# Optimization experiments

Measured on AMD Instinct MI355X. Metric: run time of the kernel, lower is better.

The kernel has to match this reference:

```python
import math
import jax, jax.numpy as jnp
import numpy as np

C = 64
GRID = 2

def _conv1x1(x, W, b):
    # 1x1 conv == channel-mixing matmul: [B,C,H,W] x [O,C] -> [B,O,H,W]
    return jnp.einsum('bchw,oc->bohw', x, W) + b[None, :, None, None]

def setup_inputs() -> dict:
    key = jax.random.key(0)
    ks = jax.random.split(key, 11)
    s = 1.0 / math.sqrt(C)
    def w(k):
        return jax.random.normal(k, (C, C), dtype=jnp.float32) * s
    def bias(k):
        return jax.random.normal(k, (C,), dtype=jnp.float32) * 0.02
    return {
        'x': jax.random.normal(ks[0], (2, C, 128, 128), dtype=jnp.float32),
        'Wq': w(ks[1]), 'bq': bias(ks[2]),
        'Wk': w(ks[3]), 'bk': bias(ks[4]),
        'Wa': w(ks[5]), 'ba': bias(ks[6]),
        'Wb': w(ks[7]), 'bb': bias(ks[8]),
        'Wo': w(ks[9]), 'bo': bias(ks[10]),
    }

def reference(x, Wq, bq, Wk, bk, Wa, ba, Wb, bb, Wo, bo):
    B, c, H, W = x.shape
    g = GRID
    rh, rw = H // g, W // g  # H,W chosen divisible by grid -> no reflect pad
    N = rh * rw
    R = g * g

    q = _conv1x1(x, Wq, bq)
    k = _conv1x1(x, Wk, bk)
    a = _conv1x1(x, Wa, ba)
    bt = _conv1x1(x, Wb, bb)

    def regionize(t):
        # [B,C,H,W] -> [B, R, C, N] with N = rh*rw row-major per region
        return t.reshape(B, c, g, rh, g, rw).transpose(0, 2, 4, 1, 3, 5).reshape(B, R, c, N)

    qr, kr, ar, br = regionize(q), regionize(k), regionize(a), regionize(bt)

    # attn[b,r,n,m] = softmax_m( q^T k / sqrt(C) )
    attn = jax.nn.softmax(jnp.einsum('brcn,brcm->brnm', qr, kr) / math.sqrt(c), axis=-1)

    # out_r = alpha @ attn + beta @ attn^T
    out = (jnp.einsum('brcj,brjm->brcm', ar, attn)
           + jnp.einsum('brcj,brmj->brcm', br, attn))

    # [B,R,C,N] -> [B,C,H,W]
    out = out.reshape(B, g, g, c, rh, rw).transpose(0, 3, 1, 4, 2, 5).reshape(B, c, H, W)
    return _conv1x1(out, Wo, bo)
```

## Files before the change

kernel.cpp:

```cpp
#include <hip/hip_runtime.h>


typedef __attribute__((ext_vector_type(8)))  short bf16x8;
typedef __attribute__((ext_vector_type(16))) float f32x16;

#define MFMA32(a, b, c) __builtin_amdgcn_mfma_f32_32x32x16_bf16(a, b, c, 0, 0, 0)

constexpr int REG_ELEMS = 4096 * 64;
constexpr size_t QP_OFF  = 0;
constexpr size_t KP_OFF  = 4u  << 20;
constexpr size_t ATL_OFF = 8u  << 20;
constexpr size_t BTL_OFF = 12u << 20;
constexpr size_t OUTP_OFF= 16u << 20;
constexpr size_t LNV_OFF = 20u << 20;

constexpr float QSCALE = 0.18033688011112042f;

__device__ __forceinline__ short f2bf(float f) {
    union { float f; unsigned u; } v; v.f = f;
    unsigned r = v.u + 0x7fffu + ((v.u >> 16) & 1u);
    return (short)(r >> 16);
}
__device__ __forceinline__ float bf2f(short s) {
    union { unsigned u; float f; } v; v.u = ((unsigned)(unsigned short)s) << 16;
    return v.f;
}
__device__ __forceinline__ unsigned fbits(float f) {
    union { float f; unsigned u; } v; v.f = f; return v.u;
}
__device__ __forceinline__ unsigned pack_trunc(float e0, float e1) {
    return __builtin_amdgcn_perm(fbits(e1), fbits(e0), 0x07060302u);
}
__device__ __forceinline__ f32x16 zero16() {
    f32x16 z;
    #pragma unroll
    for (int i = 0; i < 16; ++i) z[i] = 0.f;
    return z;
}
__device__ __forceinline__ float fexp2(float x) {
#if __has_builtin(__builtin_amdgcn_exp2f)
    return __builtin_amdgcn_exp2f(x);
#else
    return exp2f(x);
#endif
}
__device__ __forceinline__ void permswap32(unsigned& a, unsigned& b, bool hi) {
#if __has_builtin(__builtin_amdgcn_permlane32_swap)
    auto r = __builtin_amdgcn_permlane32_swap(a, b, false, false);
    a = r[0]; b = r[1];
#elif __has_builtin(__builtin_amdgcn_permlane32_swap_b32)
    auto r = __builtin_amdgcn_permlane32_swap_b32(a, b, false, false);
    a = r[0]; b = r[1];
#else
    unsigned ax = (unsigned)__shfl_xor((int)a, 32);
    unsigned bx = (unsigned)__shfl_xor((int)b, 32);
    unsigned na = hi ? bx : a;
    unsigned nb = hi ? b  : ax;
    a = na; b = nb;
#endif
}

typedef __attribute__((address_space(1))) const unsigned char as1_t;
typedef __attribute__((address_space(3))) unsigned char as3_t;
__device__ __forceinline__ void stage16(const void* g, void* l) {
    __builtin_amdgcn_global_load_lds((as1_t*)g, (as3_t*)l, 16, 0, 0);
}

__global__ __launch_bounds__(256) void k_conv_in(
    const float* __restrict__ x,
    const float* __restrict__ Wq, const float* __restrict__ bq,
    const float* __restrict__ Wk, const float* __restrict__ bk,
    const float* __restrict__ Wa, const float* __restrict__ ba,
    const float* __restrict__ Wb, const float* __restrict__ bb,
    char* __restrict__ ws)
{
    const int tid  = threadIdx.x;
    const int blk  = blockIdx.x;
    const int wseg = blk & 1;
    const int h    = (blk >> 1) & 127;
    const int b    = blk >> 8;
    const int br   = b * 4 + (h >> 6) * 2 + wseg;
    const int n0   = (h & 63) * 64;

    __shared__ float xs[64][68];
    __shared__ short trans[2][64][72];

    const float* xp = x + ((size_t)b * 64 * 16384) + (size_t)h * 128 + wseg * 64;
    #pragma unroll
    for (int r = 0; r < 4; ++r) {
        int idx = r * 256 + tid;
        int c   = idx >> 4;
        int w4  = (idx & 15) << 2;
        *(float4*)&xs[c][w4] = *(const float4*)(xp + (size_t)c * 16384 + w4);
    }
    __syncthreads();

    const int lane = tid & 63;
    const int wid  = tid >> 6;
    const int col  = lane & 31;
    const int l5   = lane >> 5;
    const int pH   = wid & 1;
    const int oH   = wid >> 1;
    const int px   = pH * 32 + col;
    const int oc   = oH * 32 + col;

    bf16x8 xhi[4], xlo[4];
    #pragma unroll
    for (int s = 0; s < 4; ++s) {
        union { bf16x8 v; short sh[8]; } uh, ul;
        #pragma unroll
        for (int e = 0; e < 8; ++e) {
            float xv = xs[s * 16 + l5 * 8 + e][px];
            short hh = f2bf(xv);
            uh.sh[e] = hh;
            ul.sh[e] = f2bf(xv - bf2f(hh));
        }
        xhi[s] = uh.v; xlo[s] = ul.v;
    }

    #pragma unroll
    for (int mat = 0; mat < 4; ++mat) {
        const float* Wsel = (mat == 0) ? Wq : (mat == 1) ? Wk : (mat == 2) ? Wa : Wb;
        const float* bsel = (mat == 0) ? bq : (mat == 1) ? bk : (mat == 2) ? ba : bb;

        bf16x8 whi[4], wlo[4];
        const float* wrow = Wsel + (size_t)oc * 64;
        #pragma unroll
        for (int s = 0; s < 4; ++s) {
            float4 f0 = *(const float4*)(wrow + s * 16 + l5 * 8);
            float4 f1 = *(const float4*)(wrow + s * 16 + l5 * 8 + 4);
            float wf[8] = { f0.x, f0.y, f0.z, f0.w, f1.x, f1.y, f1.z, f1.w };
            union { bf16x8 v; short sh[8]; } uh, ul;
            #pragma unroll
            for (int e = 0; e < 8; ++e) {
                short hh = f2bf(wf[e]);
                uh.sh[e] = hh;
                ul.sh[e] = f2bf(wf[e] - bf2f(hh));
            }
            whi[s] = uh.v; wlo[s] = ul.v;
        }

        f32x16 d = zero16();
        #pragma unroll
        for (int s = 0; s < 4; ++s) {
            d = MFMA32(xhi[s], whi[s], d);
            d = MFMA32(xhi[s], wlo[s], d);
            d = MFMA32(xlo[s], whi[s], d);
        }

        const float bias = bsel[oc];
        if (mat < 2) {
            const float sc = (mat == 0) ? QSCALE : 1.0f;
            #pragma unroll
            for (int r = 0; r < 16; ++r) {
                int pxl = pH * 32 + (r & 3) + 8 * (r >> 2) + 4 * l5;
                trans[mat][pxl][oc] = f2bf((d[r] + bias) * sc);
            }
        } else {
            short* base = (short*)(ws + (mat == 2 ? ATL_OFF : BTL_OFF))
                          + (size_t)br * REG_ELEMS;
            const int sw   = (oc >> 1) & 3;
            const int tile = (n0 >> 5) + pH;
            #pragma unroll
            for (int q = 0; q < 4; ++q) {
                short tmp4[4];
                #pragma unroll
                for (int rr = 0; rr < 4; ++rr) tmp4[rr] = f2bf(d[4 * q + rr] + bias);
                int segp = q ^ sw;
                short* p = base + (size_t)tile * 2048 + oc * 32 + segp * 8 + 4 * l5;
                *(uint2*)p = *(uint2*)tmp4;
            }
        }
    }
    __syncthreads();

    #pragma unroll
    for (int rep = 0; rep < 4; ++rep) {
        int idx  = rep * 256 + tid;
        int mat2 = idx >> 9;
        int row  = (idx >> 3) & 63;
        int seg  = idx & 7;
        short* dst = (short*)(ws + (mat2 ? KP_OFF : QP_OFF))
                     + (size_t)br * REG_ELEMS + (size_t)(n0 + row) * 64
                     + (seg ^ (row & 7)) * 8;
        *(uint4*)dst = *(uint4*)&trans[mat2][row][seg * 8];
    }
}

__global__ __launch_bounds__(256, 2) void k_stats(char* __restrict__ ws)
{
    const int tid  = threadIdx.x;
    const int br   = blockIdx.x & 7;
    const int nt   = blockIdx.x >> 3;
    const int lane = tid & 63;
    const int w    = tid >> 6;
    const int wn   = w & 1;
    const int wi   = w >> 1;
    const int col  = lane & 31;
    const int l5   = lane >> 5;

    const short* Qb  = (const short*)(ws + QP_OFF) + (size_t)br * REG_ELEMS;
    const char*  Kbb = ws + KP_OFF + (size_t)br * REG_ELEMS * 2;

    __shared__ __align__(16) char smem[17408];

    const int nrow = nt * 64 + wn * 32 + col;
    bf16x8 afr[4];
    #pragma unroll
    for (int s = 0; s < 4; ++s)
        afr[s] = *(const bf16x8*)(Qb + (size_t)nrow * 64 + (((2*s+l5) ^ (col & 7)) * 8));

    float sm[16];
    #pragma unroll
    for (int r = 0; r < 16; ++r) sm[r] = 0.f;

    {
        const char* g = Kbb + (size_t)w * 2048 + lane * 16;
        char* l = smem + w * 2048;
        stage16(g, l); stage16(g + 1024, l + 1024);
    }

    #pragma unroll 2
    for (int slab = 0; slab < 64; ++slab) {
        __syncthreads();
        if (slab + 1 < 64) {
            const char* g = Kbb + (size_t)(slab + 1) * 8192 + w * 2048 + lane * 16;
            char* l = smem + ((slab + 1) & 1) * 8192 + w * 2048;
            stage16(g, l); stage16(g + 1024, l + 1024);
        }
        const short* Ks = (const short*)(smem + (slab & 1) * 8192);
        f32x16 d = zero16();
        #pragma unroll
        for (int s = 0; s < 4; ++s) {
            bf16x8 bf = *(const bf16x8*)(Ks + (wi * 32 + col) * 64
                                         + ((2*s+l5) ^ (col & 7)) * 8);
            d = MFMA32(afr[s], bf, d);
        }
        #pragma unroll
        for (int r = 0; r < 16; ++r) sm[r] += fexp2(d[r]);
    }

    #pragma unroll
    for (int off = 1; off < 32; off <<= 1)
        #pragma unroll
        for (int r = 0; r < 16; ++r) sm[r] += __shfl_xor(sm[r], off);

    __syncthreads();
    float* Lred = (float*)(smem + 16384);
    float* Larr = (float*)(smem + 16896);
    if (col == 0) {
        #pragma unroll
        for (int r = 0; r < 16; ++r)
            Lred[w * 32 + ((r & 3) + 8 * (r >> 2) + 4 * l5)] = sm[r];
    }
    __syncthreads();
    if (tid < 64) {
        int wn2 = tid >> 5, nl = tid & 31;
        float L = Lred[wn2 * 32 + nl] + Lred[(wn2 + 2) * 32 + nl];
        float li = 1.0f / L;
        Larr[tid] = li;
        ((float*)(ws + LNV_OFF))[(size_t)br * 4096 + nt * 64 + tid] = li;
    }
    __syncthreads();

    short* Ab = (short*)(ws + ATL_OFF) + (size_t)br * REG_ELEMS + (size_t)nt * 4096;
    #pragma unroll
    for (int rep = 0; rep < 2; ++rep) {
        int id = rep * 256 + tid;
        int t = id >> 8, c = (id >> 2) & 63, s = id & 3;
        int sg = s ^ ((c >> 1) & 3);
        int jl = t * 32 + sg * 8;
        short* p = Ab + (size_t)t * 2048 + c * 32 + s * 8;
        uint4 v = *(uint4*)p;
        short* sp = (short*)&v;
        short o[8];
        #pragma unroll
        for (int e = 0; e < 8; ++e) o[e] = f2bf(bf2f(sp[e]) * Larr[jl + e]);
        *(uint4*)p = *(uint4*)o;
    }
}

__global__ __launch_bounds__(256, 2) void k_attn(char* __restrict__ ws)
{
    const int tid  = threadIdx.x;
    const int br   = blockIdx.x & 7;
    const int mt   = blockIdx.x >> 3;
    const int lane = tid & 63;
    const int w    = tid >> 6;
    const int wm   = w & 1;
    const int wj   = w >> 1;
    const int col  = lane & 31;
    const int l5   = lane >> 5;
    const bool hi  = (l5 != 0);

    const char* Qbb = ws + QP_OFF  + (size_t)br * REG_ELEMS * 2;
    const char* Kbb = ws + KP_OFF  + (size_t)br * REG_ELEMS * 2;
    const char* Abb = ws + ATL_OFF + (size_t)br * REG_ELEMS * 2;
    const char* Bbb = ws + BTL_OFF + (size_t)br * REG_ELEMS * 2;
    const float* Lnv = (const float*)(ws + LNV_OFF) + (size_t)br * 4096;
    short* OutPb    = (short*)(ws + OUTP_OFF) + (size_t)br * REG_ELEMS;

    __shared__ __align__(16) char smem[32768];

    const int mrow = mt * 64 + wm * 32 + col;
    const short* msrc = (const short*)(wj == 0 ? Kbb : Qbb) + (size_t)mrow * 64;
    bf16x8 mf[4];
    #pragma unroll
    for (int s = 0; s < 4; ++s)
        mf[s] = *(const bf16x8*)(msrc + ((2*s+l5) ^ (col & 7)) * 8);

    f32x16 accL = zero16(), accH = zero16();

    const char* gsb = (w == 0) ? Qbb : (w == 1) ? Kbb : (w == 2) ? Abb : Bbb;

    {
        const char* g = gsb + lane * 16;
        char* l = smem + w * 4096 + lane * 16;
        #pragma unroll
        for (int i = 0; i < 4; ++i) stage16(g + i * 1024, l + i * 1024);
    }

    #pragma unroll 2
    for (int slab = 0; slab < 128; ++slab) {
        __syncthreads();
        if (slab + 1 < 128) {
            const char* g = gsb + (size_t)(slab + 1) * 4096 + lane * 16;
            char* l = smem + ((slab + 1) & 1) * 16384 + w * 4096 + lane * 16;
            #pragma unroll
            for (int i = 0; i < 4; ++i) stage16(g + i * 1024, l + i * 1024);
        }
        const char* sb = smem + (slab & 1) * 16384;
        const short* js = (const short*)(sb + (wj == 0 ? 0 : 4096));
        const short* ts = (const short*)(sb + (wj == 0 ? 8192 : 12288));

        f32x16 d = zero16();
        #pragma unroll
        for (int s = 0; s < 4; ++s) {
            bf16x8 a = *(const bf16x8*)(js + col * 64 + ((2*s+l5) ^ (col & 7)) * 8);
            d = MFMA32(a, mf[s], d);
        }

        unsigned Wp[8];
        #pragma unroll
        for (int q = 0; q < 4; ++q) {
            Wp[2*q]   = pack_trunc(fexp2(d[4*q]),   fexp2(d[4*q+1]));
            Wp[2*q+1] = pack_trunc(fexp2(d[4*q+2]), fexp2(d[4*q+3]));
        }

        #pragma unroll
        for (int k16 = 0; k16 < 2; ++k16) {
            unsigned u0 = Wp[4*k16+0], u1 = Wp[4*k16+1];
            unsigned u2 = Wp[4*k16+2], u3 = Wp[4*k16+3];
            permswap32(u0, u2, hi);
            permswap32(u1, u3, hi);
            union { uint4 u; bf16x8 v; } fr;
            fr.u.x = u0; fr.u.y = u1; fr.u.z = u2; fr.u.w = u3;

            const int swz = ((2*k16 + l5) ^ ((col >> 1) & 3)) * 8;
            bf16x8 bL = *(const bf16x8*)(ts + col * 32 + swz);
            bf16x8 bH = *(const bf16x8*)(ts + (col + 32) * 32 + swz);
            accL = MFMA32(fr.v, bL, accL);
            accH = MFMA32(fr.v, bH, accH);
        }
    }

    __syncthreads();
    float* red = (float*)smem;
    if (wj == 0) {
        #pragma unroll
        for (int r = 0; r < 16; ++r) {
            int ml = wm * 32 + (r & 3) + 8 * (r >> 2) + 4 * l5;
            red[ml * 68 + col]      = accL[r];
            red[ml * 68 + 32 + col] = accH[r];
        }
    }
    __syncthreads();
    if (wj == 1) {
        #pragma unroll
        for (int r = 0; r < 16; ++r) {
            int ml = wm * 32 + (r & 3) + 8 * (r >> 2) + 4 * l5;
            float li = Lnv[mt * 64 + ml];
            red[ml * 68 + col]      += li * accL[r];
            red[ml * 68 + 32 + col] += li * accH[r];
        }
    }
    __syncthreads();
    {
        const int m  = tid >> 2;
        const int c0 = (tid & 3) * 16;
        const float* rp = red + m * 68 + c0;
        uint4 p0, p1;
        p0.x = pack_trunc(rp[0],  rp[1]);  p0.y = pack_trunc(rp[2],  rp[3]);
        p0.z = pack_trunc(rp[4],  rp[5]);  p0.w = pack_trunc(rp[6],  rp[7]);
        p1.x = pack_trunc(rp[8],  rp[9]);  p1.y = pack_trunc(rp[10], rp[11]);
        p1.z = pack_trunc(rp[12], rp[13]); p1.w = pack_trunc(rp[14], rp[15]);
        short* orow = OutPb + (size_t)(mt * 64 + m) * 64 + c0;
        *(uint4*)orow       = p0;
        *(uint4*)(orow + 8) = p1;
    }
}

__global__ __launch_bounds__(64) void k_conv_out(
    const char* __restrict__ ws,
    const float* __restrict__ Wo, const float* __restrict__ bo,
    float* __restrict__ out)
{
    const int lane = threadIdx.x;
    const int br   = blockIdx.x & 7;
    const int nt   = blockIdx.x >> 3;
    const int col  = lane & 31;
    const int l5   = lane >> 5;

    const short* OutPb = (const short*)(ws + OUTP_OFF) + (size_t)br * REG_ELEMS;

    bf16x8 afr[4];
    const short* arow = OutPb + (size_t)(nt * 32 + col) * 64 + l5 * 8;
    #pragma unroll
    for (int s = 0; s < 4; ++s) afr[s] = *(const bf16x8*)(arow + s * 16);

    bf16x8 bw[2][4];
    #pragma unroll
    for (int oh = 0; oh < 2; ++oh) {
        const float* wrow = Wo + (size_t)(oh * 32 + col) * 64 + l5 * 8;
        #pragma unroll
        for (int s = 0; s < 4; ++s) {
            float4 f0 = *(const float4*)(wrow + s * 16);
            float4 f1 = *(const float4*)(wrow + s * 16 + 4);
            union { bf16x8 v; short sh[8]; } u;
            u.sh[0] = f2bf(f0.x); u.sh[1] = f2bf(f0.y);
            u.sh[2] = f2bf(f0.z); u.sh[3] = f2bf(f0.w);
            u.sh[4] = f2bf(f1.x); u.sh[5] = f2bf(f1.y);
            u.sh[6] = f2bf(f1.z); u.sh[7] = f2bf(f1.w);
            bw[oh][s] = u.v;
        }
    }

    f32x16 d0 = zero16(), d1 = zero16();
    #pragma unroll
    for (int s = 0; s < 4; ++s) {
        d0 = MFMA32(afr[s], bw[0][s], d0);
        d1 = MFMA32(afr[s], bw[1][s], d1);
    }

    const int b  = br >> 2;
    const int gi = (br >> 1) & 1;
    const int gj = br & 1;

    #pragma unroll
    for (int oh = 0; oh < 2; ++oh) {
        const int oc = oh * 32 + col;
        const float bias = bo[oc];
        const f32x16& d = oh ? d1 : d0;
        #pragma unroll
        for (int q = 0; q < 4; ++q) {
            int nloc = 8 * q + 4 * l5;
            int nreg = nt * 32 + nloc;
            int wp   = nreg & 63;
            int ip   = nreg >> 6;
            float4 v = make_float4(d[4*q+0] + bias, d[4*q+1] + bias,
                                   d[4*q+2] + bias, d[4*q+3] + bias);
            float* op = out + ((size_t)(b * 64 + oc)) * 16384
                        + (size_t)(gi * 64 + ip) * 128 + gj * 64 + wp;
            *(float4*)op = v;
        }
    }
}

extern "C" void kernel_launch(void* const* d_in, const int* in_sizes, int n_in,
                              void* d_out, int out_size, void* d_ws, size_t ws_size,
                              hipStream_t stream)
{
    const float* x  = (const float*)d_in[0];
    const float* Wq = (const float*)d_in[1];
    const float* bq = (const float*)d_in[2];
    const float* Wk = (const float*)d_in[3];
    const float* bk = (const float*)d_in[4];
    const float* Wa = (const float*)d_in[5];
    const float* ba = (const float*)d_in[6];
    const float* Wb = (const float*)d_in[7];
    const float* bb = (const float*)d_in[8];
    const float* Wo = (const float*)d_in[9];
    const float* bo = (const float*)d_in[10];
    char* ws   = (char*)d_ws;
    float* out = (float*)d_out;

    hipLaunchKernelGGL(k_conv_in,  dim3(512),  dim3(256), 0, stream,
                       x, Wq, bq, Wk, bk, Wa, ba, Wb, bb, ws);
    hipLaunchKernelGGL(k_stats,    dim3(512),  dim3(256), 0, stream, ws);
    hipLaunchKernelGGL(k_attn,     dim3(512),  dim3(256), 0, stream, ws);
    hipLaunchKernelGGL(k_conv_out, dim3(1024), dim3(64),  0, stream,
                       ws, Wo, bo, out);
}
```

Before: 206.1 us.

## Split softmax row-sum stats over key halves and batch conv_out waves

The stats kernel now splits each region's 4096 key columns into two halves handled by separate blocks, doubling the grid to 1024 blocks. Each block writes partial row sums, and a new k_ascale kernel combines them, computes the reciprocal and rescales the stored A tiles. k_conv_out is regrouped from 1024 single-wave blocks into 256 blocks of four waves each. The aim is better GPU occupancy and parallelism in the exp-heavy stats pass, at the cost of one extra kernel launch and a round trip of the partial sums through global memory.

```diff
diff --git a/kernel.cpp b/kernel.cpp
--- a/kernel.cpp
+++ b/kernel.cpp
@@ -7,12 +7,13 @@
 #define MFMA32(a, b, c) __builtin_amdgcn_mfma_f32_32x32x16_bf16(a, b, c, 0, 0, 0)
 
 constexpr int REG_ELEMS = 4096 * 64;
-constexpr size_t QP_OFF  = 0;
-constexpr size_t KP_OFF  = 4u  << 20;
-constexpr size_t ATL_OFF = 8u  << 20;
-constexpr size_t BTL_OFF = 12u << 20;
-constexpr size_t OUTP_OFF= 16u << 20;
-constexpr size_t LNV_OFF = 20u << 20;
+constexpr size_t QP_OFF    = 0;
+constexpr size_t KP_OFF    = 4u  << 20;
+constexpr size_t ATL_OFF   = 8u  << 20;
+constexpr size_t BTL_OFF   = 12u << 20;
+constexpr size_t OUTP_OFF  = 16u << 20;
+constexpr size_t LNV_OFF   = 20u << 20;
+constexpr size_t LPART_OFF = (20u << 20) + (128u << 10);
 
 constexpr float QSCALE = 0.18033688011112042f;
 
@@ -191,7 +192,8 @@
 {
     const int tid  = threadIdx.x;
     const int br   = blockIdx.x & 7;
-    const int nt   = blockIdx.x >> 3;
+    const int nt   = (blockIdx.x >> 3) & 63;
+    const int ms   = blockIdx.x >> 9;
     const int lane = tid & 63;
     const int w    = tid >> 6;
     const int wn   = w & 1;
@@ -200,9 +202,10 @@
     const int l5   = lane >> 5;
 
     const short* Qb  = (const short*)(ws + QP_OFF) + (size_t)br * REG_ELEMS;
-    const char*  Kbb = ws + KP_OFF + (size_t)br * REG_ELEMS * 2;
-
-    __shared__ __align__(16) char smem[17408];
+    const char*  Kbb = ws + KP_OFF + (size_t)br * REG_ELEMS * 2
+                       + (size_t)ms * 262144;
+
+    __shared__ __align__(16) char smem[16896];
 
     const int nrow = nt * 64 + wn * 32 + col;
     bf16x8 afr[4];
@@ -221,9 +224,9 @@
     }
 
     #pragma unroll 2
-    for (int slab = 0; slab < 64; ++slab) {
+    for (int slab = 0; slab < 32; ++slab) {
         __syncthreads();
-        if (slab + 1 < 64) {
+        if (slab + 1 < 32) {
             const char* g = Kbb + (size_t)(slab + 1) * 8192 + w * 2048 + lane * 16;
             char* l = smem + ((slab + 1) & 1) * 8192 + w * 2048;
             stage16(g, l); stage16(g + 1024, l + 1024);
@@ -247,7 +250,6 @@
 
     __syncthreads();
     float* Lred = (float*)(smem + 16384);
-    float* Larr = (float*)(smem + 16896);
     if (col == 0) {
         #pragma unroll
         for (int r = 0; r < 16; ++r)
@@ -257,9 +259,25 @@
     if (tid < 64) {
         int wn2 = tid >> 5, nl = tid & 31;
         float L = Lred[wn2 * 32 + nl] + Lred[(wn2 + 2) * 32 + nl];
-        float li = 1.0f / L;
+        ((float*)(ws + LPART_OFF))[(size_t)ms * 32768 + (size_t)br * 4096
+                                   + nt * 64 + tid] = L;
+    }
+}
+
+__global__ __launch_bounds__(256) void k_ascale(char* __restrict__ ws)
+{
+    const int tid = threadIdx.x;
+    const int br  = blockIdx.x & 7;
+    const int nt  = blockIdx.x >> 3;
+
+    __shared__ float Larr[64];
+
+    if (tid < 64) {
+        const float* Lp = (const float*)(ws + LPART_OFF);
+        const size_t idx = (size_t)br * 4096 + nt * 64 + tid;
+        float li = 1.0f / (Lp[idx] + Lp[32768 + idx]);
         Larr[tid] = li;
-        ((float*)(ws + LNV_OFF))[(size_t)br * 4096 + nt * 64 + tid] = li;
+        ((float*)(ws + LNV_OFF))[idx] = li;
     }
     __syncthreads();
 
@@ -400,14 +418,17 @@
     }
 }
 
-__global__ __launch_bounds__(64) void k_conv_out(
+__global__ __launch_bounds__(256) void k_conv_out(
     const char* __restrict__ ws,
     const float* __restrict__ Wo, const float* __restrict__ bo,
     float* __restrict__ out)
 {
-    const int lane = threadIdx.x;
-    const int br   = blockIdx.x & 7;
-    const int nt   = blockIdx.x >> 3;
+    const int tid  = threadIdx.x;
+    const int lane = tid & 63;
+    const int sub  = tid >> 6;
+    const int blk  = blockIdx.x;
+    const int br   = blk & 7;
+    const int nt   = (blk >> 3) * 4 + sub;
     const int col  = lane & 31;
     const int l5   = lane >> 5;
 
@@ -486,8 +507,9 @@
 
     hipLaunchKernelGGL(k_conv_in,  dim3(512),  dim3(256), 0, stream,
                        x, Wq, bq, Wk, bk, Wa, ba, Wb, bb, ws);
-    hipLaunchKernelGGL(k_stats,    dim3(512),  dim3(256), 0, stream, ws);
+    hipLaunchKernelGGL(k_stats,    dim3(1024), dim3(256), 0, stream, ws);
+    hipLaunchKernelGGL(k_ascale,   dim3(512),  dim3(256), 0, stream, ws);
     hipLaunchKernelGGL(k_attn,     dim3(512),  dim3(256), 0, stream, ws);
-    hipLaunchKernelGGL(k_conv_out, dim3(1024), dim3(64),  0, stream,
+    hipLaunchKernelGGL(k_conv_out, dim3(256),  dim3(256), 0, stream,
                        ws, Wo, bo, out);
 }
```

Measured after the change: 205.2 us. About the same (-0.5%).
